# Kernel optimization log

Measured on AMD Instinct MI355X. Metric: run time of the kernel, lower is better.

Reference implementation:

```python
import jax, jax.numpy as jnp
import numpy as np

T, B, H, I = 2048, 32, 1024, 1024

def setup_inputs() -> dict:
    key = jax.random.key(0)
    k1, k2, k3 = jax.random.split(key, 3)
    x = jax.random.normal(k1, (T, B, I), dtype=jnp.float32)
    # torch RNN default init: uniform(-1/sqrt(H), 1/sqrt(H))
    bound = 1.0 / np.sqrt(H)
    w_ih = jax.random.uniform(k2, (H, I), dtype=jnp.float32, minval=-bound, maxval=bound)
    b_ih = jnp.zeros((H,), dtype=jnp.float32)  # zeroed in IndRNN.__init__
    b_hh = jnp.zeros((H,), dtype=jnp.float32)
    # diagonal recurrent weight, uniform(-1, 1) per the module
    u = jax.random.uniform(k3, (H,), dtype=jnp.float32, minval=-1.0, maxval=1.0)
    return {"x": x, "w_ih": w_ih, "b_ih": b_ih, "b_hh": b_hh, "u": u}

def reference(x, w_ih, b_ih, b_hh, u):
    # Precompute input projection for all timesteps: [T, B, H]
    pre = jnp.einsum('tbi,hi->tbh', x, w_ih) + (b_ih + b_hh)

    def step(h, p):
        h_new = jax.nn.relu(p + u * h)  # diagonal recurrence: elementwise
        return h_new, h_new

    h0 = jnp.zeros((B, H), dtype=x.dtype)
    h_last, ys = jax.lax.scan(step, h0, pre)
    # Match torch.nn.RNN output: (output [T,B,H], h_n [1,B,H])
    return ys, h_last[None]
```

## Files before the change

### kernel.cpp

```cpp
#include <hip/hip_runtime.h>

#define T_DIM 2048
#define B_DIM 32
#define H_DIM 1024
#define I_DIM 1024
#define M_DIM (T_DIM * B_DIM)
#define K_DIM I_DIM
#define N_DIM H_DIM
#define YS_ELEMS (M_DIM * H_DIM)
#define BH (B_DIM * H_DIM)

typedef unsigned short u16;
typedef __attribute__((ext_vector_type(8))) short bf16x8;
typedef __attribute__((ext_vector_type(16))) float f32x16;

__device__ __forceinline__ u16 f2bf(float f) {
  union { float f; unsigned u; } c; c.f = f;
  return (u16)((c.u + 0x7fffu + ((c.u >> 16) & 1u)) >> 16);
}
__device__ __forceinline__ float bf2f(u16 s) {
  union { float f; unsigned u; } c; c.u = ((unsigned)s) << 16;
  return c.f;
}

__global__ __launch_bounds__(256) void split_kernel(
    const float* __restrict__ x, u16* __restrict__ hi, u16* __restrict__ lo, int n4) {
  int i = blockIdx.x * 256 + threadIdx.x;
  if (i >= n4) return;
  float4 v = ((const float4*)x)[i];
  ushort4 h, l;
  h.x = f2bf(v.x); l.x = f2bf(v.x - bf2f(h.x));
  h.y = f2bf(v.y); l.y = f2bf(v.y - bf2f(h.y));
  h.z = f2bf(v.z); l.z = f2bf(v.z - bf2f(h.z));
  h.w = f2bf(v.w); l.w = f2bf(v.w - bf2f(h.w));
  ((ushort4*)hi)[i] = h;
  ((ushort4*)lo)[i] = l;
}

__device__ __forceinline__ void gload_lds16(const u16* g, u16* l) {
  __builtin_amdgcn_global_load_lds(
      (const __attribute__((address_space(1))) void*)g,
      (__attribute__((address_space(3))) void*)l, 16, 0, 0);
}

__global__ __launch_bounds__(256, 2) void gemm_split(
    const u16* __restrict__ Ah, const u16* __restrict__ Al,
    const u16* __restrict__ Bh, const u16* __restrict__ Bl,
    float* __restrict__ C) {
  __shared__ u16 sAh[128 * 32], sAl[128 * 32], sBh[128 * 32], sBl[128 * 32];

  const int bid = blockIdx.x;
  const int grp = bid >> 8;
  const int r = bid & 255;
  const int n0 = (r >> 5) * 128;
  const int m0 = ((grp << 5) + (r & 31)) * 128;

  const int tid = threadIdx.x;
  const int wave = tid >> 6;
  const int lane = tid & 63;

  const int srow = tid >> 2;
  const int skofs = (tid & 3) * 8;

  const u16* gAh0 = Ah + (size_t)(m0 + srow) * K_DIM + skofs;
  const u16* gAh1 = gAh0 + (size_t)64 * K_DIM;
  const u16* gAl0 = Al + (size_t)(m0 + srow) * K_DIM + skofs;
  const u16* gAl1 = gAl0 + (size_t)64 * K_DIM;
  const u16* gBh0 = Bh + (size_t)(n0 + srow) * K_DIM + skofs;
  const u16* gBh1 = gBh0 + (size_t)64 * K_DIM;
  const u16* gBl0 = Bl + (size_t)(n0 + srow) * K_DIM + skofs;
  const u16* gBl1 = gBl0 + (size_t)64 * K_DIM;

  const int wofs = wave * 512;

  const int wm = (wave & 1) * 64;
  const int wn = (wave >> 1) * 64;
  const int cl = lane & 31;
  const int kh8 = (lane >> 5) * 8;

  f32x16 acc[2][2] = {};

  for (int k0 = 0; k0 < K_DIM; k0 += 32) {
    __syncthreads();
    gload_lds16(gAh0 + k0, sAh + wofs);
    gload_lds16(gAh1 + k0, sAh + wofs + 2048);
    gload_lds16(gAl0 + k0, sAl + wofs);
    gload_lds16(gAl1 + k0, sAl + wofs + 2048);
    gload_lds16(gBh0 + k0, sBh + wofs);
    gload_lds16(gBh1 + k0, sBh + wofs + 2048);
    gload_lds16(gBl0 + k0, sBl + wofs);
    gload_lds16(gBl1 + k0, sBl + wofs + 2048);
    __syncthreads();

    bf16x8 ah[2][2], al[2][2], bh[2][2], bl[2][2];
#pragma unroll
    for (int i = 0; i < 2; ++i)
#pragma unroll
      for (int s = 0; s < 2; ++s) {
        ah[i][s] = *(const bf16x8*)(sAh + (wm + i * 32 + cl) * 32 + s * 16 + kh8);
        al[i][s] = *(const bf16x8*)(sAl + (wm + i * 32 + cl) * 32 + s * 16 + kh8);
        bh[i][s] = *(const bf16x8*)(sBh + (wn + i * 32 + cl) * 32 + s * 16 + kh8);
        bl[i][s] = *(const bf16x8*)(sBl + (wn + i * 32 + cl) * 32 + s * 16 + kh8);
      }
#pragma unroll
    for (int s = 0; s < 2; ++s)
#pragma unroll
      for (int i = 0; i < 2; ++i)
#pragma unroll
        for (int j = 0; j < 2; ++j) {
          acc[i][j] = __builtin_amdgcn_mfma_f32_32x32x16_bf16(ah[i][s], bh[j][s], acc[i][j], 0, 0, 0);
          acc[i][j] = __builtin_amdgcn_mfma_f32_32x32x16_bf16(ah[i][s], bl[j][s], acc[i][j], 0, 0, 0);
          acc[i][j] = __builtin_amdgcn_mfma_f32_32x32x16_bf16(al[i][s], bh[j][s], acc[i][j], 0, 0, 0);
        }
  }

  const int rh = (lane >> 5) * 4;
#pragma unroll
  for (int i = 0; i < 2; ++i)
#pragma unroll
    for (int j = 0; j < 2; ++j) {
      const int col = n0 + wn + j * 32 + cl;
      const size_t rb = (size_t)(m0 + wm + i * 32 + rh);
#pragma unroll
      for (int rr = 0; rr < 16; ++rr)
        C[(rb + (rr & 3) + 8 * (rr >> 2)) * N_DIM + col] = acc[i][j][rr];
    }
}

__global__ __launch_bounds__(64) void scan_kernel(
    float* __restrict__ yio, float* __restrict__ hlast,
    const float* __restrict__ bih, const float* __restrict__ bhh,
    const float* __restrict__ u) {
  const int j = blockIdx.x * 64 + threadIdx.x;
  const int hc = j & (H_DIM - 1);
  const float uu = u[hc];
  const float bias = bih[hc] + bhh[hc];
  float h = 0.f;
  float* p = yio + j;
  constexpr int UN = 32;
  float bufA[UN], bufB[UN];
#pragma unroll
  for (int i = 0; i < UN; ++i) bufA[i] = p[(size_t)i * BH];
#pragma unroll 1
  for (int t0 = 0; t0 < T_DIM; t0 += 2 * UN) {
#pragma unroll
    for (int i = 0; i < UN; ++i) bufB[i] = p[(size_t)(t0 + UN + i) * BH];
#pragma unroll
    for (int i = 0; i < UN; ++i) {
      float v = bufA[i] + bias + uu * h;
      h = v > 0.f ? v : 0.f;
      p[(size_t)(t0 + i) * BH] = h;
    }
    if (t0 + 2 * UN < T_DIM) {
#pragma unroll
      for (int i = 0; i < UN; ++i) bufA[i] = p[(size_t)(t0 + 2 * UN + i) * BH];
    }
#pragma unroll
    for (int i = 0; i < UN; ++i) {
      float v = bufB[i] + bias + uu * h;
      h = v > 0.f ? v : 0.f;
      p[(size_t)(t0 + UN + i) * BH] = h;
    }
  }
  hlast[j] = h;
}

extern "C" void kernel_launch(void* const* d_in, const int* in_sizes, int n_in,
                              void* d_out, int out_size, void* d_ws, size_t ws_size,
                              hipStream_t stream) {
  const float* x   = (const float*)d_in[0];
  const float* w   = (const float*)d_in[1];
  const float* bih = (const float*)d_in[2];
  const float* bhh = (const float*)d_in[3];
  const float* u   = (const float*)d_in[4];
  float* out = (float*)d_out;

  u16* xh = (u16*)d_ws;
  u16* xl = xh + (size_t)YS_ELEMS;
  u16* wh = xl + (size_t)YS_ELEMS;
  u16* wl = wh + (size_t)(H_DIM * I_DIM);

  split_kernel<<<YS_ELEMS / 4 / 256, 256, 0, stream>>>(x, xh, xl, YS_ELEMS / 4);
  split_kernel<<<(H_DIM * I_DIM) / 4 / 256, 256, 0, stream>>>(w, wh, wl, (H_DIM * I_DIM) / 4);
  gemm_split<<<(M_DIM / 128) * (N_DIM / 128), 256, 0, stream>>>(xh, xl, wh, wl, out);
  scan_kernel<<<BH / 64, 64, 0, stream>>>(out, out + (size_t)YS_ELEMS, bih, bhh, u);
}
```

Measured before the change: 936.7 us.

## Rewrite split-bf16 GEMM with 256x256 tiles, double-buffered LDS pipeline, swizzle

The split-bf16 GEMM moves to 512-thread blocks computing 256x256 output tiles. It uses double-buffered 128KB shared memory with XOR-swizzled layout, interleaves async global-to-LDS staging with MFMA quarters using explicit waitcnt and barriers, and raises MFMA priority. Block ids are remapped for locality. This aims to hide load latency and raise reuse per staged byte, at the cost of far more LDS and register pressure, which may cut occupancy. The scan unroll is also doubled.

Result: slower. 1.021 ms (+9.0%).

```diff
diff --git a/kernel.cpp b/kernel.cpp
--- a/kernel.cpp
+++ b/kernel.cpp
@@ -43,84 +43,161 @@
       (__attribute__((address_space(3))) void*)l, 16, 0, 0);
 }
 
-__global__ __launch_bounds__(256, 2) void gemm_split(
-    const u16* __restrict__ Ah, const u16* __restrict__ Al,
-    const u16* __restrict__ Bh, const u16* __restrict__ Bl,
-    float* __restrict__ C) {
-  __shared__ u16 sAh[128 * 32], sAl[128 * 32], sBh[128 * 32], sBl[128 * 32];
-
-  const int bid = blockIdx.x;
-  const int grp = bid >> 8;
-  const int r = bid & 255;
-  const int n0 = (r >> 5) * 128;
-  const int m0 = ((grp << 5) + (r & 31)) * 128;
+#define XOFF  ((unsigned)YS_ELEMS)
+#define WOFF  (2u * (unsigned)YS_ELEMS)
+#define WLOFF (WOFF + (unsigned)(H_DIM * I_DIM))
+
+#define WAITV(N) asm volatile("s_waitcnt vmcnt(" #N ")" ::: "memory")
+#define BARX() do { asm volatile("" ::: "memory"); \
+                    __builtin_amdgcn_s_barrier(); \
+                    asm volatile("" ::: "memory"); } while (0)
+
+#define STAGE(k, NB) gload_lds16(ws0 + gofs[k] + ks, \
+    smem + ((NB) << 15) + ((k) < 4 ? 0 : 16384) + (((k) & 3) << 12) + (wave << 9))
+
+#define RD_APAIR(P, AB) { \
+  _Pragma("unroll") for (int i2_ = 0; i2_ < 2; ++i2_) { \
+    const u16* ap_ = (AB) + aRowOff[2 * (P) + i2_]; \
+    _Pragma("unroll") for (int s_ = 0; s_ < 2; ++s_) { \
+      aH[i2_][s_] = *(const bf16x8*)(ap_ + soH[s_]); \
+      aL[i2_][s_] = *(const bf16x8*)(ap_ + soL[s_]); \
+    } } }
+
+#define RD_B(J, BB) { \
+  const u16* bp_ = (BB) + bRowOff[J]; \
+  _Pragma("unroll") for (int s_ = 0; s_ < 2; ++s_) { \
+    bh2[J][s_] = *(const bf16x8*)(bp_ + soH[s_]); \
+    bl2[J][s_] = *(const bf16x8*)(bp_ + soL[s_]); \
+  } }
+
+#define MFMA_Q(P, J) { \
+  __builtin_amdgcn_s_setprio(1); \
+  _Pragma("unroll") for (int s_ = 0; s_ < 2; ++s_) \
+  _Pragma("unroll") for (int i2_ = 0; i2_ < 2; ++i2_) { \
+    acc[2*(P)+i2_][J] = __builtin_amdgcn_mfma_f32_32x32x16_bf16(aH[i2_][s_], bh2[J][s_], acc[2*(P)+i2_][J], 0, 0, 0); \
+    acc[2*(P)+i2_][J] = __builtin_amdgcn_mfma_f32_32x32x16_bf16(aH[i2_][s_], bl2[J][s_], acc[2*(P)+i2_][J], 0, 0, 0); \
+    acc[2*(P)+i2_][J] = __builtin_amdgcn_mfma_f32_32x32x16_bf16(aL[i2_][s_], bh2[J][s_], acc[2*(P)+i2_][J], 0, 0, 0); \
+  } \
+  __builtin_amdgcn_s_setprio(0); }
+
+#define DO_TILE_MAIN(AB, BB, NB) { \
+  RD_APAIR(0, AB) RD_B(0, BB) \
+  STAGE(0, NB); STAGE(1, NB); \
+  WAITV(4); BARX(); \
+  MFMA_Q(0, 0) BARX(); \
+  RD_B(1, BB) \
+  STAGE(4, NB); STAGE(5, NB); \
+  WAITV(4); BARX(); \
+  MFMA_Q(0, 1) BARX(); \
+  RD_APAIR(1, AB) \
+  STAGE(6, NB); STAGE(7, NB); \
+  BARX(); \
+  MFMA_Q(1, 0) BARX(); \
+  STAGE(2, NB); STAGE(3, NB); \
+  WAITV(4); BARX(); \
+  MFMA_Q(1, 1) BARX(); \
+  ks += 32; }
+
+#define DO_TILE_LAST(AB, BB) { \
+  RD_APAIR(0, AB) RD_B(0, BB) \
+  WAITV(2); BARX(); \
+  MFMA_Q(0, 0) BARX(); \
+  RD_B(1, BB) \
+  WAITV(0); BARX(); \
+  MFMA_Q(0, 1) BARX(); \
+  RD_APAIR(1, AB) \
+  BARX(); \
+  MFMA_Q(1, 0) BARX(); \
+  BARX(); \
+  MFMA_Q(1, 1) BARX(); }
+
+__global__ __launch_bounds__(512, 2) void gemm_split(
+    const u16* __restrict__ ws0, float* __restrict__ C) {
+  __shared__ u16 smem[65536];
 
   const int tid = threadIdx.x;
   const int wave = tid >> 6;
   const int lane = tid & 63;
-
-  const int srow = tid >> 2;
-  const int skofs = (tid & 3) * 8;
-
-  const u16* gAh0 = Ah + (size_t)(m0 + srow) * K_DIM + skofs;
-  const u16* gAh1 = gAh0 + (size_t)64 * K_DIM;
-  const u16* gAl0 = Al + (size_t)(m0 + srow) * K_DIM + skofs;
-  const u16* gAl1 = gAl0 + (size_t)64 * K_DIM;
-  const u16* gBh0 = Bh + (size_t)(n0 + srow) * K_DIM + skofs;
-  const u16* gBh1 = gBh0 + (size_t)64 * K_DIM;
-  const u16* gBl0 = Bl + (size_t)(n0 + srow) * K_DIM + skofs;
-  const u16* gBl1 = gBl0 + (size_t)64 * K_DIM;
-
-  const int wofs = wave * 512;
-
-  const int wm = (wave & 1) * 64;
-  const int wn = (wave >> 1) * 64;
   const int cl = lane & 31;
-  const int kh8 = (lane >> 5) * 8;
-
-  f32x16 acc[2][2] = {};
-
-  for (int k0 = 0; k0 < K_DIM; k0 += 32) {
-    __syncthreads();
-    gload_lds16(gAh0 + k0, sAh + wofs);
-    gload_lds16(gAh1 + k0, sAh + wofs + 2048);
-    gload_lds16(gAl0 + k0, sAl + wofs);
-    gload_lds16(gAl1 + k0, sAl + wofs + 2048);
-    gload_lds16(gBh0 + k0, sBh + wofs);
-    gload_lds16(gBh1 + k0, sBh + wofs + 2048);
-    gload_lds16(gBl0 + k0, sBl + wofs);
-    gload_lds16(gBl1 + k0, sBl + wofs + 2048);
-    __syncthreads();
-
-    bf16x8 ah[2][2], al[2][2], bh[2][2], bl[2][2];
-#pragma unroll
-    for (int i = 0; i < 2; ++i)
-#pragma unroll
-      for (int s = 0; s < 2; ++s) {
-        ah[i][s] = *(const bf16x8*)(sAh + (wm + i * 32 + cl) * 32 + s * 16 + kh8);
-        al[i][s] = *(const bf16x8*)(sAl + (wm + i * 32 + cl) * 32 + s * 16 + kh8);
-        bh[i][s] = *(const bf16x8*)(sBh + (wn + i * 32 + cl) * 32 + s * 16 + kh8);
-        bl[i][s] = *(const bf16x8*)(sBl + (wn + i * 32 + cl) * 32 + s * 16 + kh8);
-      }
-#pragma unroll
-    for (int s = 0; s < 2; ++s)
-#pragma unroll
-      for (int i = 0; i < 2; ++i)
-#pragma unroll
-        for (int j = 0; j < 2; ++j) {
-          acc[i][j] = __builtin_amdgcn_mfma_f32_32x32x16_bf16(ah[i][s], bh[j][s], acc[i][j], 0, 0, 0);
-          acc[i][j] = __builtin_amdgcn_mfma_f32_32x32x16_bf16(ah[i][s], bl[j][s], acc[i][j], 0, 0, 0);
-          acc[i][j] = __builtin_amdgcn_mfma_f32_32x32x16_bf16(al[i][s], bh[j][s], acc[i][j], 0, 0, 0);
-        }
-  }
-
-  const int rh = (lane >> 5) * 4;
-#pragma unroll
-  for (int i = 0; i < 2; ++i)
+  const int kh = lane >> 5;
+  const int sx = lane & 7;
+
+  const int bid = blockIdx.x;
+  const int id = ((bid & 7) << 7) | (bid >> 3);
+  const int m0 = (id >> 2) << 8;
+  const int n0 = (id & 3) << 8;
+
+  unsigned gofs[8];
+#pragma unroll
+  for (int k = 0; k < 8; ++k) {
+    const int p = ((k & 3) << 13) | (wave << 10) | (lane << 4);
+    const int rho = p >> 7;
+    const int slot = (p >> 4) & 7;
+    const int cc = slot ^ (rho & 7);
+    const int pl = cc >> 2;
+    const int c = cc & 3;
+    int r; unsigned base;
+    if (k < 4) {
+      const int g = rho >> 6;
+      r = m0 + (((g & 1) << 7) | ((g >> 1) << 6) | (rho & 63));
+      base = pl ? XOFF : 0u;
+    } else {
+      const int q = rho >> 5;
+      const int blk = ((q & 3) << 1) | (q >> 2);
+      r = n0 + ((blk << 5) | (rho & 31));
+      base = pl ? WLOFF : WOFF;
+    }
+    gofs[k] = base + (unsigned)r * 1024u + (unsigned)(c << 3);
+  }
+
+  const int wmH = wave >> 2;
+  const int wn = (wave & 3) << 6;
+  int aRowOff[4];
+#pragma unroll
+  for (int i = 0; i < 4; ++i)
+    aRowOff[i] = ((((i >> 1) << 7) | (wmH << 6) | ((i & 1) << 5) | cl) << 6);
+  int bRowOff[2];
+#pragma unroll
+  for (int j = 0; j < 2; ++j) {
+    const int b = (wn >> 5) + j;
+    bRowOff[j] = ((((b & 1) << 7) | ((b >> 1) << 5) | cl) << 6);
+  }
+  int soH[2], soL[2];
+#pragma unroll
+  for (int s = 0; s < 2; ++s) {
+    soH[s] = ((((s << 1) | kh)) ^ sx) << 3;
+    soL[s] = (((4 | (s << 1) | kh)) ^ sx) << 3;
+  }
+
+  const u16* a0 = smem;
+  const u16* b0 = smem + 16384;
+  const u16* a1 = smem + 32768;
+  const u16* b1 = smem + 49152;
+
+  bf16x8 aH[2][2], aL[2][2], bh2[2][2], bl2[2][2];
+  f32x16 acc[4][2] = {};
+
+  int ks = 0;
+  STAGE(0, 0); STAGE(1, 0); STAGE(4, 0); STAGE(5, 0);
+  STAGE(6, 0); STAGE(7, 0); STAGE(2, 0); STAGE(3, 0);
+  ks = 32;
+  WAITV(4); BARX();
+
+#pragma unroll 1
+  for (int it = 0; it < 15; ++it) {
+    DO_TILE_MAIN(a0, b0, 1)
+    DO_TILE_MAIN(a1, b1, 0)
+  }
+  DO_TILE_MAIN(a0, b0, 1)
+  DO_TILE_LAST(a1, b1)
+
+  const int rh = (lane >> 5) << 2;
+#pragma unroll
+  for (int i = 0; i < 4; ++i)
 #pragma unroll
     for (int j = 0; j < 2; ++j) {
       const int col = n0 + wn + j * 32 + cl;
-      const size_t rb = (size_t)(m0 + wm + i * 32 + rh);
+      const size_t rb = (size_t)(m0 + wmH * 128 + i * 32 + rh);
 #pragma unroll
       for (int rr = 0; rr < 16; ++rr)
         C[(rb + (rr & 3) + 8 * (rr >> 2)) * N_DIM + col] = acc[i][j][rr];
@@ -137,7 +214,7 @@
   const float bias = bih[hc] + bhh[hc];
   float h = 0.f;
   float* p = yio + j;
-  constexpr int UN = 32;
+  constexpr int UN = 64;
   float bufA[UN], bufB[UN];
 #pragma unroll
   for (int i = 0; i < UN; ++i) bufA[i] = p[(size_t)i * BH];
@@ -182,6 +259,6 @@
 
   split_kernel<<<YS_ELEMS / 4 / 256, 256, 0, stream>>>(x, xh, xl, YS_ELEMS / 4);
   split_kernel<<<(H_DIM * I_DIM) / 4 / 256, 256, 0, stream>>>(w, wh, wl, (H_DIM * I_DIM) / 4);
-  gemm_split<<<(M_DIM / 128) * (N_DIM / 128), 256, 0, stream>>>(xh, xl, wh, wl, out);
+  gemm_split<<<1024, 512, 0, stream>>>((const u16*)d_ws, out);
   scan_kernel<<<BH / 64, 64, 0, stream>>>(out, out + (size_t)YS_ELEMS, bih, bhh, u);
 }
```

## Fuse x bf16 hi/lo split into GEMM with swizzled double-buffered LDS

Applied to the files above, without the earlier changes.

Drops the separate pass that splits x into bf16 hi/lo planes. The GEMM now reads fp32 x directly, splits it in registers and writes it into an XOR-swizzled shared-memory tile, which removes a full write and re-read of a 2x-sized intermediate. The W tiles are double-buffered with async global-to-LDS loads and the next x slice is prefetched into registers, with raised MFMA priority and an occupancy hint of 3. The scan unroll also grows from 32 to 64, which raises register pressure in exchange for deeper load prefetch.

After: 878.9 us. -6.2%, faster.

```diff
diff --git a/kernel.cpp b/kernel.cpp
--- a/kernel.cpp
+++ b/kernel.cpp
@@ -43,75 +43,144 @@
       (__attribute__((address_space(3))) void*)l, 16, 0, 0);
 }
 
-__global__ __launch_bounds__(256, 2) void gemm_split(
-    const u16* __restrict__ Ah, const u16* __restrict__ Al,
-    const u16* __restrict__ Bh, const u16* __restrict__ Bl,
-    float* __restrict__ C) {
-  __shared__ u16 sAh[128 * 32], sAl[128 * 32], sBh[128 * 32], sBl[128 * 32];
-
-  const int bid = blockIdx.x;
-  const int grp = bid >> 8;
-  const int r = bid & 255;
-  const int n0 = (r >> 5) * 128;
-  const int m0 = ((grp << 5) + (r & 31)) * 128;
+#define WAITV0()    asm volatile("s_waitcnt vmcnt(0)" ::: "memory")
+#define WAITLGKM0() asm volatile("s_waitcnt lgkmcnt(0)" ::: "memory")
+#define BARX() do { asm volatile("" ::: "memory"); \
+                    __builtin_amdgcn_s_barrier(); \
+                    asm volatile("" ::: "memory"); } while (0)
+
+__global__ __launch_bounds__(256, 3) void gemm_fused(
+    const float* __restrict__ X, const u16* __restrict__ Wh,
+    const u16* __restrict__ Wl, float* __restrict__ C) {
+  __shared__ u16 sA[128 * 64];
+  __shared__ u16 sB[2][128 * 64];
 
   const int tid = threadIdx.x;
   const int wave = tid >> 6;
   const int lane = tid & 63;
-
-  const int srow = tid >> 2;
-  const int skofs = (tid & 3) * 8;
-
-  const u16* gAh0 = Ah + (size_t)(m0 + srow) * K_DIM + skofs;
-  const u16* gAh1 = gAh0 + (size_t)64 * K_DIM;
-  const u16* gAl0 = Al + (size_t)(m0 + srow) * K_DIM + skofs;
-  const u16* gAl1 = gAl0 + (size_t)64 * K_DIM;
-  const u16* gBh0 = Bh + (size_t)(n0 + srow) * K_DIM + skofs;
-  const u16* gBh1 = gBh0 + (size_t)64 * K_DIM;
-  const u16* gBl0 = Bl + (size_t)(n0 + srow) * K_DIM + skofs;
-  const u16* gBl1 = gBl0 + (size_t)64 * K_DIM;
-
-  const int wofs = wave * 512;
-
-  const int wm = (wave & 1) * 64;
-  const int wn = (wave >> 1) * 64;
   const int cl = lane & 31;
-  const int kh8 = (lane >> 5) * 8;
+  const int kh = lane >> 5;
+  const int sx = lane & 7;
+
+  const int bid = blockIdx.x;
+  const int grp = bid >> 8;
+  const int rr_ = bid & 255;
+  const int n0 = (rr_ >> 5) * 128;
+  const int m0 = ((grp << 5) + (rr_ & 31)) * 128;
+
+  const u16* bsrc[4];
+#pragma unroll
+  for (int q = 0; q < 4; ++q) {
+    const int rho = (q << 5) | (tid >> 3);
+    const int slot = tid & 7;
+    const int cc = slot ^ (rho & 7);
+    const int pl = cc >> 2;
+    const int c = cc & 3;
+    bsrc[q] = (pl ? Wl : Wh) + (size_t)(n0 + rho) * K_DIM + (c << 3);
+  }
+
+  const int ar = tid >> 1;
+  const int aseg = tid & 1;
+  const float* xsrc = X + (size_t)(m0 + ar) * K_DIM + (aseg << 4);
+  int awofs[2][2];
+#pragma unroll
+  for (int pl = 0; pl < 2; ++pl)
+#pragma unroll
+    for (int cq = 0; cq < 2; ++cq) {
+      const int cc = (pl << 2) | (aseg << 1) | cq;
+      awofs[pl][cq] = (ar << 6) + ((cc ^ (ar & 7)) << 3);
+    }
+
+  const int wm = (wave & 1) << 6;
+  const int wn = (wave >> 1) << 6;
+  int aRow[2], bRow[2];
+#pragma unroll
+  for (int i = 0; i < 2; ++i) {
+    aRow[i] = (wm + (i << 5) + cl) << 6;
+    bRow[i] = (wn + (i << 5) + cl) << 6;
+  }
+  int soH[2], soL[2];
+#pragma unroll
+  for (int s = 0; s < 2; ++s) {
+    soH[s] = ((((s << 1) | kh)) ^ sx) << 3;
+    soL[s] = (((4 | (s << 1) | kh)) ^ sx) << 3;
+  }
 
   f32x16 acc[2][2] = {};
 
+  float4 xv0 = ((const float4*)xsrc)[0];
+  float4 xv1 = ((const float4*)xsrc)[1];
+  float4 xv2 = ((const float4*)xsrc)[2];
+  float4 xv3 = ((const float4*)xsrc)[3];
+#pragma unroll
+  for (int q = 0; q < 4; ++q)
+    gload_lds16(bsrc[q], &sB[0][(q << 11) + (wave << 9)]);
+
+#pragma unroll 1
   for (int k0 = 0; k0 < K_DIM; k0 += 32) {
-    __syncthreads();
-    gload_lds16(gAh0 + k0, sAh + wofs);
-    gload_lds16(gAh1 + k0, sAh + wofs + 2048);
-    gload_lds16(gAl0 + k0, sAl + wofs);
-    gload_lds16(gAl1 + k0, sAl + wofs + 2048);
-    gload_lds16(gBh0 + k0, sBh + wofs);
-    gload_lds16(gBh1 + k0, sBh + wofs + 2048);
-    gload_lds16(gBl0 + k0, sBl + wofs);
-    gload_lds16(gBl1 + k0, sBl + wofs + 2048);
-    __syncthreads();
-
-    bf16x8 ah[2][2], al[2][2], bh[2][2], bl[2][2];
-#pragma unroll
-    for (int i = 0; i < 2; ++i)
-#pragma unroll
-      for (int s = 0; s < 2; ++s) {
-        ah[i][s] = *(const bf16x8*)(sAh + (wm + i * 32 + cl) * 32 + s * 16 + kh8);
-        al[i][s] = *(const bf16x8*)(sAl + (wm + i * 32 + cl) * 32 + s * 16 + kh8);
-        bh[i][s] = *(const bf16x8*)(sBh + (wn + i * 32 + cl) * 32 + s * 16 + kh8);
-        bl[i][s] = *(const bf16x8*)(sBl + (wn + i * 32 + cl) * 32 + s * 16 + kh8);
+    const int buf = (k0 >> 5) & 1;
+    BARX();
+    WAITV0();
+
+    {
+      float xf[16];
+      *(float4*)(xf + 0) = xv0;  *(float4*)(xf + 4) = xv1;
+      *(float4*)(xf + 8) = xv2;  *(float4*)(xf + 12) = xv3;
+      u16 hh[16], ll[16];
+#pragma unroll
+      for (int e = 0; e < 16; ++e) {
+        hh[e] = f2bf(xf[e]);
+        ll[e] = f2bf(xf[e] - bf2f(hh[e]));
       }
 #pragma unroll
-    for (int s = 0; s < 2; ++s)
+      for (int cq = 0; cq < 2; ++cq) {
+        bf16x8 hv, lv;
+#pragma unroll
+        for (int e = 0; e < 8; ++e) {
+          hv[e] = (short)hh[cq * 8 + e];
+          lv[e] = (short)ll[cq * 8 + e];
+        }
+        *(bf16x8*)(sA + awofs[0][cq]) = hv;
+        *(bf16x8*)(sA + awofs[1][cq]) = lv;
+      }
+    }
+
+    if (k0 + 32 < K_DIM) {
+      const float* xs = xsrc + k0 + 32;
+      xv0 = ((const float4*)xs)[0];
+      xv1 = ((const float4*)xs)[1];
+      xv2 = ((const float4*)xs)[2];
+      xv3 = ((const float4*)xs)[3];
+#pragma unroll
+      for (int q = 0; q < 4; ++q)
+        gload_lds16(bsrc[q] + k0 + 32, &sB[buf ^ 1][(q << 11) + (wave << 9)]);
+    }
+
+    WAITLGKM0();
+    BARX();
+
+    const u16* bb = &sB[buf][0];
+#pragma unroll
+    for (int s = 0; s < 2; ++s) {
+      bf16x8 ah[2], al[2], bh[2], bl[2];
+#pragma unroll
+      for (int i = 0; i < 2; ++i) {
+        ah[i] = *(const bf16x8*)(sA + aRow[i] + soH[s]);
+        al[i] = *(const bf16x8*)(sA + aRow[i] + soL[s]);
+        bh[i] = *(const bf16x8*)(bb + bRow[i] + soH[s]);
+        bl[i] = *(const bf16x8*)(bb + bRow[i] + soL[s]);
+      }
+      __builtin_amdgcn_s_setprio(1);
 #pragma unroll
       for (int i = 0; i < 2; ++i)
 #pragma unroll
         for (int j = 0; j < 2; ++j) {
-          acc[i][j] = __builtin_amdgcn_mfma_f32_32x32x16_bf16(ah[i][s], bh[j][s], acc[i][j], 0, 0, 0);
-          acc[i][j] = __builtin_amdgcn_mfma_f32_32x32x16_bf16(ah[i][s], bl[j][s], acc[i][j], 0, 0, 0);
-          acc[i][j] = __builtin_amdgcn_mfma_f32_32x32x16_bf16(al[i][s], bh[j][s], acc[i][j], 0, 0, 0);
+          acc[i][j] = __builtin_amdgcn_mfma_f32_32x32x16_bf16(ah[i], bh[j], acc[i][j], 0, 0, 0);
+          acc[i][j] = __builtin_amdgcn_mfma_f32_32x32x16_bf16(ah[i], bl[j], acc[i][j], 0, 0, 0);
+          acc[i][j] = __builtin_amdgcn_mfma_f32_32x32x16_bf16(al[i], bh[j], acc[i][j], 0, 0, 0);
         }
+      __builtin_amdgcn_s_setprio(0);
+    }
   }
 
   const int rh = (lane >> 5) * 4;
@@ -137,7 +206,7 @@
   const float bias = bih[hc] + bhh[hc];
   float h = 0.f;
   float* p = yio + j;
-  constexpr int UN = 32;
+  constexpr int UN = 64;
   float bufA[UN], bufB[UN];
 #pragma unroll
   for (int i = 0; i < UN; ++i) bufA[i] = p[(size_t)i * BH];
@@ -175,13 +244,10 @@
   const float* u   = (const float*)d_in[4];
   float* out = (float*)d_out;
 
-  u16* xh = (u16*)d_ws;
-  u16* xl = xh + (size_t)YS_ELEMS;
-  u16* wh = xl + (size_t)YS_ELEMS;
+  u16* wh = (u16*)d_ws;
   u16* wl = wh + (size_t)(H_DIM * I_DIM);
 
-  split_kernel<<<YS_ELEMS / 4 / 256, 256, 0, stream>>>(x, xh, xl, YS_ELEMS / 4);
   split_kernel<<<(H_DIM * I_DIM) / 4 / 256, 256, 0, stream>>>(w, wh, wl, (H_DIM * I_DIM) / 4);
-  gemm_split<<<(M_DIM / 128) * (N_DIM / 128), 256, 0, stream>>>(xh, xl, wh, wl, out);
+  gemm_fused<<<4096, 256, 0, stream>>>(x, wh, wl, out);
   scan_kernel<<<BH / 64, 64, 0, stream>>>(out, out + (size_t)YS_ELEMS, bih, bhh, u);
 }
```
